# Optimization experiments

Measured on AMD Instinct MI355X. Metric: run time of the kernel, lower is better.

The kernel has to match this reference:

```python
import jax, jax.numpy as jnp
import numpy as np

BETA = 1.0
GAMMA = 0.25


def setup_inputs() -> dict:
    key = jax.random.key(0)
    ks = jax.random.split(key, 8)
    N, D_in, D_h, D_z = 65536, 1024, 512, 256
    s = lambda fan_in: 1.0 / np.sqrt(fan_in)
    return {
        "x": jax.random.normal(ks[0], (N, D_in), jnp.float32),
        "eW1": jax.random.normal(ks[1], (D_in, D_h), jnp.float32) * s(D_in),
        "eb1": jnp.zeros((D_h,), jnp.float32),
        "eW2": jax.random.normal(ks[2], (D_h, D_z), jnp.float32) * s(D_h),
        "eb2": jnp.zeros((D_z,), jnp.float32),
        "dW1": jax.random.normal(ks[3], (D_z, D_h), jnp.float32) * s(D_z),
        "db1": jnp.zeros((D_h,), jnp.float32),
        "dW2": jax.random.normal(ks[4], (D_h, D_in), jnp.float32) * s(D_h),
        "db2": jnp.zeros((D_in,), jnp.float32),
        "C0": jax.random.normal(ks[5], (1024, D_z), jnp.float32),
        "C1": jax.random.normal(ks[6], (512, D_z), jnp.float32),
        "C2": jax.random.normal(ks[7], (256, D_z), jnp.float32),
    }


def _nearest_idx(r, C):
    # argmin of squared euclidean distance == argmin of cdist(p=2)
    r = jax.lax.stop_gradient(r)
    d2 = jnp.sum(r * r, -1, keepdims=True) - 2.0 * (r @ C.T) + jnp.sum(C * C, -1)
    return jnp.argmin(d2, axis=-1)


def reference(x, eW1, eb1, eW2, eb2, dW1, db1, dW2, db2, C0, C1, C2):
    sg = jax.lax.stop_gradient
    # encoder: Linear -> GELU (exact) -> Linear
    z = jax.nn.gelu(x @ eW1 + eb1, approximate=False) @ eW2 + eb2
    residual = z
    output = jnp.zeros_like(z)
    losses = []
    for C in (C0, C1, C2):
        idx = _nearest_idx(residual, sg(C))
        q = C[idx]                                    # [N, 256] gather
        z2c = jnp.mean((residual - sg(q)) ** 2)       # commit input to code
        c2z = jnp.mean((sg(residual) - q) ** 2)       # move code to input
        losses.append(BETA * c2z + GAMMA * z2c)
        output = output + q
        residual = residual - q
    # straight-through: z + sg(zq) - sg(z)
    h = z + sg(output) - sg(z)
    out = jax.nn.gelu(h @ dW1 + db1, approximate=False) @ dW2 + db2
    recon_loss = jnp.mean((out - x) ** 2)
    return jnp.stack([recon_loss] + losses)  # [4]: recon, commit0, commit1, commit2
```

## Files before the change

kernel.cpp:

```cpp
#include <hip/hip_runtime.h>
#include <cstddef>


typedef __attribute__((ext_vector_type(8))) __bf16 bf16x8;
typedef __attribute__((ext_vector_type(4))) float f32x4;
typedef unsigned short u16;

__device__ __forceinline__ u16 f2bf(float f) {
    unsigned u = __float_as_uint(f);
    u += 0x7fffu + ((u >> 16) & 1u);
    return (u16)(u >> 16);
}
__device__ __forceinline__ float bf2f(u16 b) {
    return __uint_as_float((unsigned)b << 16);
}
__device__ __forceinline__ float gelu_exact(float v) {
    return 0.5f * v * (1.0f + erff(v * 0.7071067811865475f));
}
__device__ __forceinline__ void gload16(const void* g, void* l) {
    __builtin_amdgcn_global_load_lds(
        (const __attribute__((address_space(1))) void*)g,
        (__attribute__((address_space(3))) void*)l, 16, 0, 0);
}
__device__ __forceinline__ f32x4 mfma_bf16(bf16x8 a, bf16x8 b, f32x4 c) {
    return __builtin_amdgcn_mfma_f32_16x16x32_bf16(a, b, c, 0, 0, 0);
}

__global__ __launch_bounds__(256)
void prep_x(const float* __restrict__ x, u16* __restrict__ xbf)
{
    const size_t total = (size_t)65536 * 1024;
    const size_t step  = (size_t)gridDim.x * 256 * 8;
    for (size_t i = ((size_t)blockIdx.x * 256 + threadIdx.x) * 8; i < total; i += step) {
        float4 v0 = *(const float4*)&x[i];
        float4 v1 = *(const float4*)&x[i + 4];
        uint4 o;
        o.x = (unsigned)f2bf(v0.x) | ((unsigned)f2bf(v0.y) << 16);
        o.y = (unsigned)f2bf(v0.z) | ((unsigned)f2bf(v0.w) << 16);
        o.z = (unsigned)f2bf(v1.x) | ((unsigned)f2bf(v1.y) << 16);
        o.w = (unsigned)f2bf(v1.z) | ((unsigned)f2bf(v1.w) << 16);
        *(uint4*)&xbf[i] = o;
    }
}

__global__ __launch_bounds__(256)
void prep_weights(const float* __restrict__ eW1, const float* __restrict__ eW2,
                  const float* __restrict__ dW1, const float* __restrict__ dW2,
                  u16* __restrict__ eW1t, u16* __restrict__ eW2t,
                  u16* __restrict__ dW1t, u16* __restrict__ dW2t)
{
    const int b = blockIdx.x, t = threadIdx.x;
    if (b < 2048) {
        int e = b * 256 + t;
        int n = e >> 10, k = e & 1023;
        eW1t[e] = f2bf(eW1[(size_t)k * 512 + n]);
    } else if (b < 2560) {
        int e = (b - 2048) * 256 + t;
        int n = e >> 9, k = e & 511;
        eW2t[e] = f2bf(eW2[(size_t)k * 256 + n]);
    } else if (b < 3072) {
        int e = (b - 2560) * 256 + t;
        int n = e >> 8, k = e & 255;
        dW1t[e] = f2bf(dW1[(size_t)k * 512 + n]);
    } else {
        int e = (b - 3072) * 256 + t;
        int n = e >> 9, k = e & 511;
        dW2t[e] = f2bf(dW2[(size_t)k * 1024 + n]);
    }
}

__global__ __launch_bounds__(256)
void cb_prep(const float* __restrict__ C0, const float* __restrict__ C1,
             const float* __restrict__ C2, u16* __restrict__ Cbf,
             float* __restrict__ cnorm)
{
    __shared__ float red[256];
    const int code = blockIdx.x, t = threadIdx.x;
    const float* C;
    int local;
    if (code < 1024)      { C = C0; local = code; }
    else if (code < 1536) { C = C1; local = code - 1024; }
    else                  { C = C2; local = code - 1536; }
    const float v = C[(size_t)local * 256 + t];
    Cbf[(size_t)code * 256 + t] = f2bf(v);
    red[t] = v * v;
    __syncthreads();
    for (int s = 128; s; s >>= 1) { if (t < s) red[t] += red[t + s]; __syncthreads(); }
    if (t == 0) cnorm[code] = red[0];
}

template <int EPI>
__global__ __launch_bounds__(512, 2)
void gemm_mfma(const u16* __restrict__ A, const u16* __restrict__ Bt,
               const float* __restrict__ bias, u16* __restrict__ Obf,
               float* __restrict__ Of, const u16* __restrict__ Xbf,
               float* __restrict__ lossOut, int N, int K, int ntn,
               float lossScale)
{
    __shared__ __align__(16) u16 SA[2][2][8192];
    __shared__ __align__(16) u16 SB[2][2][8192];

    const int nwg = gridDim.x;
    const int bid = blockIdx.x;
    const int wg  = (bid & 7) * (nwg >> 3) + (bid >> 3);
    const int brow = (wg / ntn) * 256;
    const int bcol = (wg % ntn) * 256;

    const int t    = threadIdx.x;
    const int lane = t & 63;
    const int wid  = t >> 6;
    const int wrow = (wid >> 2) * 128;
    const int wcol = (wid & 3) * 64;
    const int lrow = lane & 15, g = lane >> 4;

    const int nt = K >> 6;

    f32x4 acc[8][4];
#pragma unroll
    for (int m = 0; m < 8; ++m)
#pragma unroll
        for (int n = 0; n < 4; ++n) acc[m][n] = (f32x4)0.f;

    auto stage_half = [&](const u16* __restrict__ src, int row0, int Ts,
                          int kh, char* region) {
#pragma unroll
        for (int it = 0; it < 2; ++it) {
            const int d  = (it * 512 + t) * 16;
            const int R  = d >> 6;
            const int cs = ((d >> 4) & 3) ^ ((R >> 1) & 3);
            gload16(&src[(size_t)(row0 + R) * K + Ts * 64 + kh * 32 + cs * 8],
                    region + d);
        }
    };

    stage_half(A,  brow, 0, 0, (char*)&SA[0][0][0]);
    stage_half(Bt, bcol, 0, 0, (char*)&SB[0][0][0]);
    stage_half(A,  brow, 0, 1, (char*)&SA[0][1][0]);
    stage_half(Bt, bcol, 0, 1, (char*)&SB[0][1][0]);
    stage_half(A,  brow, 1, 0, (char*)&SA[1][0][0]);
    stage_half(Bt, bcol, 1, 0, (char*)&SB[1][0][0]);
    asm volatile("s_waitcnt vmcnt(8)" ::: "memory");
    __builtin_amdgcn_s_barrier();

    bf16x8 bfr[4];

#define PHASE(MH, KK, DO_B, STAGE_CODE)                                        \
    {                                                                          \
        bf16x8 a_[4];                                                          \
        _Pragma("unroll")                                                      \
        for (int mi = 0; mi < 4; ++mi) {                                       \
            const int R = wrow + ((MH) * 4 + mi) * 16 + lrow;                  \
            a_[mi] = *(const bf16x8*)((const char*)&SA[d][KK][0]               \
                      + R * 64 + ((g ^ ((R >> 1) & 3)) << 4));                 \
        }                                                                      \
        if (DO_B) {                                                            \
            _Pragma("unroll")                                                  \
            for (int n = 0; n < 4; ++n) {                                      \
                const int R = wcol + n * 16 + lrow;                            \
                bfr[n] = *(const bf16x8*)((const char*)&SB[d][KK][0]           \
                          + R * 64 + ((g ^ ((R >> 1) & 3)) << 4));             \
            }                                                                  \
        }                                                                      \
        STAGE_CODE;                                                            \
        if (T >= nt - 2) asm volatile("s_waitcnt vmcnt(0)" ::: "memory");      \
        else             asm volatile("s_waitcnt vmcnt(8)" ::: "memory");      \
        __builtin_amdgcn_s_barrier();                                          \
        __builtin_amdgcn_s_setprio(1);                                         \
        _Pragma("unroll")                                                      \
        for (int mi = 0; mi < 4; ++mi)                                         \
            _Pragma("unroll")                                                  \
            for (int n = 0; n < 4; ++n)                                        \
                acc[(MH) * 4 + mi][n] =                                        \
                    mfma_bf16(a_[mi], bfr[n], acc[(MH) * 4 + mi][n]);          \
        __builtin_amdgcn_s_setprio(0);                                         \
        __builtin_amdgcn_s_barrier();                                          \
    }

    for (int T = 0; T < nt; ++T) {
        const int d = T & 1;
        PHASE(0, 0, 1,
              if (T + 1 < nt) stage_half(A, brow, T + 1, 1,
                                         (char*)&SA[(T + 1) & 1][1][0]));
        PHASE(1, 0, 0,
              if (T + 1 < nt) stage_half(Bt, bcol, T + 1, 1,
                                         (char*)&SB[(T + 1) & 1][1][0]));
        PHASE(0, 1, 1,
              if (T + 2 < nt) stage_half(A, brow, T + 2, 0,
                                         (char*)&SA[T & 1][0][0]));
        PHASE(1, 1, 0,
              if (T + 2 < nt) stage_half(Bt, bcol, T + 2, 0,
                                         (char*)&SB[T & 1][0][0]));
    }
#undef PHASE

    int   colN[4];
    float bn[4];
#pragma unroll
    for (int n = 0; n < 4; ++n) {
        colN[n] = bcol + wcol + n * 16 + lrow;
        bn[n]   = bias[colN[n]];
    }

    if (EPI == 0) {
#pragma unroll
        for (int m = 0; m < 8; ++m) {
            const int rowb = brow + wrow + m * 16 + (lane >> 4) * 4;
#pragma unroll
            for (int n = 0; n < 4; ++n)
#pragma unroll
                for (int j = 0; j < 4; ++j)
                    Obf[(size_t)(rowb + j) * N + colN[n]] =
                        f2bf(gelu_exact(acc[m][n][j] + bn[n]));
        }
    } else if (EPI == 1) {
#pragma unroll
        for (int m = 0; m < 8; ++m) {
            const int rowb = brow + wrow + m * 16 + (lane >> 4) * 4;
#pragma unroll
            for (int n = 0; n < 4; ++n)
#pragma unroll
                for (int j = 0; j < 4; ++j)
                    Of[(size_t)(rowb + j) * N + colN[n]] = acc[m][n][j] + bn[n];
        }
    } else if (EPI == 3) {
#pragma unroll
        for (int m = 0; m < 8; ++m) {
            const int rowb = brow + wrow + m * 16 + (lane >> 4) * 4;
#pragma unroll
            for (int n = 0; n < 4; ++n)
#pragma unroll
                for (int j = 0; j < 4; ++j)
                    Obf[(size_t)(rowb + j) * N + colN[n]] =
                        f2bf(acc[m][n][j] + bn[n]);
        }
    } else {
        float partial = 0.f;
#pragma unroll
        for (int m = 0; m < 8; ++m) {
            const int rowb = brow + wrow + m * 16 + (lane >> 4) * 4;
#pragma unroll
            for (int n = 0; n < 4; ++n)
#pragma unroll
                for (int j = 0; j < 4; ++j) {
                    const float o = acc[m][n][j] + bn[n];
                    const float d = o - bf2f(Xbf[(size_t)(rowb + j) * N + colN[n]]);
                    partial = fmaf(d, d, partial);
                }
        }
        __syncthreads();
        float* red = (float*)&SA[0][0][0];
        red[t] = partial;
        __syncthreads();
        for (int s = 256; s; s >>= 1) { if (t < s) red[t] += red[t + s]; __syncthreads(); }
        if (t == 0) atomicAdd(lossOut, red[0] * lossScale);
    }
}

__global__ __launch_bounds__(512, 4)
void vq_mfma(const u16* __restrict__ Zbf, const u16* __restrict__ Cbf,
             const float* __restrict__ cnorm,
             const float* __restrict__ C0, const float* __restrict__ C1,
             const float* __restrict__ C2,
             u16* __restrict__ ZQ, float* __restrict__ lossOut)
{
    __shared__ __align__(16) char pool[66560];
    __shared__ float redv[64][2];
    __shared__ int   redi[64][2];
    __shared__ int   idxs[3][64];
    __shared__ float lred[8];

    u16 (*Rb)[264] = (u16 (*)[264])(pool + 32768);

    const int t    = threadIdx.x;
    const int lane = t & 63;
    const int wid  = t >> 6;
    const int rg   = wid & 3;
    const int cg   = wid >> 2;
    const int lrow = lane & 15, g = lane >> 4;
    const int col  = t & 255;
    const int rh   = t >> 8;
    const int brow = blockIdx.x * 64;

    float R[32];
#pragma unroll
    for (int r = 0; r < 32; ++r)
        R[r] = bf2f(Zbf[(size_t)(brow + rh * 32 + r) * 256 + col]);

    const float* Cf[3]  = {C0, C1, C2};
    const int ncodes[3] = {1024, 512, 256};
    const int coff[3]   = {0, 1024, 1536};
    const float lscale  = 1.25f / (65536.0f * 256.0f);

    const int cr = cg * 16 + lrow;

    for (int stage = 0; stage < 3; ++stage) {
        const u16*   Cb  = Cbf + (size_t)coff[stage] * 256;
        const float* cns = cnorm + coff[stage];
        const int ntile  = ncodes[stage] >> 5;

        auto stageC = [&](int tile) {
            char* region = pool + (size_t)(tile % 3) * 16384;
#pragma unroll
            for (int it = 0; it < 2; ++it) {
                const int d   = (it * 512 + t) * 16;
                const int row = d >> 9;
                const int kb  = d & 511;
                const int kbs = kb ^ ((row & 7) << 4);
                gload16(&Cb[(size_t)(tile * 32 + row) * 256 + (kbs >> 1)],
                        region + d);
            }
        };

        stageC(0);
        if (ntile > 1) stageC(1);
#pragma unroll
        for (int r = 0; r < 32; ++r) Rb[rh * 32 + r][col] = f2bf(R[r]);
        __syncthreads();

        bf16x8 a[8];
#pragma unroll
        for (int ks = 0; ks < 8; ++ks)
            a[ks] = *(const bf16x8*)&Rb[rg * 16 + lrow][ks * 32 + g * 8];
        __syncthreads();

        float best[4]; int bidx[4];
#pragma unroll
        for (int j = 0; j < 4; ++j) { best[j] = 3.0e38f; bidx[j] = 0; }

#pragma unroll 1
        for (int tile = 0; tile < ntile; ++tile) {
            if (tile >= 1) {
                if (tile + 1 < ntile) asm volatile("s_waitcnt vmcnt(2)" ::: "memory");
                else                  asm volatile("s_waitcnt vmcnt(0)" ::: "memory");
                __builtin_amdgcn_s_barrier();
            }
            if (tile + 2 < ntile) stageC(tile + 2);

            const char* Cbuf = pool + (size_t)(tile % 3) * 16384;
            const int   code = tile * 32 + cr;
            const float cn   = cns[code];
            f32x4 acc = (f32x4)0.f;
            __builtin_amdgcn_s_setprio(1);
#pragma unroll
            for (int ks = 0; ks < 8; ++ks) {
                const int kb = (ks * 64 + g * 16) ^ ((cr & 7) << 4);
                bf16x8 b = *(const bf16x8*)(Cbuf + cr * 512 + kb);
                acc = mfma_bf16(a[ks], b, acc);
            }
            __builtin_amdgcn_s_setprio(0);
#pragma unroll
            for (int j = 0; j < 4; ++j) {
                const float s = fmaf(-2.0f, acc[j], cn);
                if (s < best[j]) { best[j] = s; bidx[j] = code; }
            }
        }

#pragma unroll
        for (int j = 0; j < 4; ++j) {
            float v = best[j]; int i = bidx[j];
#pragma unroll
            for (int d = 1; d < 16; d <<= 1) {
                const float ov = __shfl_xor(v, d);
                const int   oi = __shfl_xor(i, d);
                if (ov < v || (ov == v && oi < i)) { v = ov; i = oi; }
            }
            if (lrow == 0) {
                redv[rg * 16 + g * 4 + j][cg] = v;
                redi[rg * 16 + g * 4 + j][cg] = i;
            }
        }
        __syncthreads();
        if (t < 64) {
            float v = redv[t][0]; int i = redi[t][0];
            const float ov = redv[t][1]; const int oi = redi[t][1];
            if (ov < v || (ov == v && oi < i)) { v = ov; i = oi; }
            idxs[stage][t] = i;
        }
        __syncthreads();

        const float* Cfs = Cf[stage];
        float partial = 0.f;
#pragma unroll
        for (int r = 0; r < 32; ++r) {
            const float q  = Cfs[(size_t)idxs[stage][rh * 32 + r] * 256 + col];
            const float rn = R[r] - q;
            R[r] = rn;
            partial = fmaf(rn, rn, partial);
        }
#pragma unroll
        for (int d = 32; d; d >>= 1) partial += __shfl_down(partial, d);
        if (lane == 0) lred[wid] = partial;
        __syncthreads();
        if (t == 0) {
            float s = 0.f;
#pragma unroll
            for (int w2 = 0; w2 < 8; ++w2) s += lred[w2];
            atomicAdd(&lossOut[1 + stage], s * lscale);
        }
        __syncthreads();
    }

#pragma unroll
    for (int r = 0; r < 32; ++r) {
        const int row = rh * 32 + r;
        const float zq = C0[(size_t)idxs[0][row] * 256 + col]
                       + C1[(size_t)idxs[1][row] * 256 + col]
                       + C2[(size_t)idxs[2][row] * 256 + col];
        ZQ[(size_t)(brow + row) * 256 + col] = f2bf(zq);
    }
}

extern "C" void kernel_launch(void* const* d_in, const int* in_sizes, int n_in,
                              void* d_out, int out_size, void* d_ws, size_t ws_size,
                              hipStream_t stream)
{
    const float* x   = (const float*)d_in[0];
    const float* eW1 = (const float*)d_in[1];
    const float* eb1 = (const float*)d_in[2];
    const float* eW2 = (const float*)d_in[3];
    const float* eb2 = (const float*)d_in[4];
    const float* dW1 = (const float*)d_in[5];
    const float* db1 = (const float*)d_in[6];
    const float* dW2 = (const float*)d_in[7];
    const float* db2 = (const float*)d_in[8];
    const float* C0  = (const float*)d_in[9];
    const float* C1  = (const float*)d_in[10];
    const float* C2  = (const float*)d_in[11];
    float* out = (float*)d_out;

    char* w = (char*)d_ws;
    u16*   H1   = (u16*)(w);
    u16*   Zbf  = (u16*)(w + ((size_t)64 << 20));
    u16*   ZQ   = (u16*)(w + ((size_t)128 << 20));
    u16*   H2   = (u16*)(w + ((size_t)160 << 20));
    u16*   xbf  = (u16*)(w + ((size_t)230 << 20));
    u16*   eW1t = (u16*)(w + ((size_t)224 << 20));
    u16*   eW2t = (u16*)(w + ((size_t)225 << 20));
    u16*   dW1t = (u16*)(w + ((size_t)226 << 20));
    u16*   dW2t = (u16*)(w + ((size_t)227 << 20));
    u16*   Cbf  = (u16*)(w + ((size_t)228 << 20));
    float* cn   = (float*)(w + ((size_t)229 << 20));

    hipMemsetAsync(d_out, 0, 4 * sizeof(float), stream);

    prep_x<<<4096, 256, 0, stream>>>(x, xbf);
    prep_weights<<<5120, 256, 0, stream>>>(eW1, eW2, dW1, dW2, eW1t, eW2t, dW1t, dW2t);
    cb_prep<<<1792, 256, 0, stream>>>(C0, C1, C2, Cbf, cn);

    gemm_mfma<0><<<512, 512, 0, stream>>>(
        xbf, eW1t, eb1, H1, nullptr, nullptr, nullptr, 512, 1024, 2, 0.f);
    gemm_mfma<3><<<256, 512, 0, stream>>>(
        H1, eW2t, eb2, Zbf, nullptr, nullptr, nullptr, 256, 512, 1, 0.f);
    vq_mfma<<<1024, 512, 0, stream>>>(Zbf, Cbf, cn, C0, C1, C2, ZQ, out);
    gemm_mfma<0><<<512, 512, 0, stream>>>(
        ZQ, dW1t, db1, H2, nullptr, nullptr, nullptr, 512, 256, 2, 0.f);
    gemm_mfma<2><<<1024, 512, 0, stream>>>(
        H2, dW2t, db2, nullptr, nullptr, xbf, out, 1024, 512, 4,
        1.0f / (65536.0f * 1024.0f));
}
```

Before: 549.9 us.

## Halve VQ block size so each wave computes two row tiles sharing codebook fragments

The VQ kernel now uses 256 threads (4 waves) instead of 512. Each wave handles 32 rows via two 16-row MFMA tiles that share each codebook B fragment loaded from LDS, and each thread keeps 64 residual values in registers. The goal is to halve LDS reads of the codebook per MFMA and raise MFMA density per wave. The cost is higher register pressure, lower launch-bound occupancy (2 blocks) and fewer waves to hide latency in the gather and residual phases.

```diff
diff --git a/kernel.cpp b/kernel.cpp
--- a/kernel.cpp
+++ b/kernel.cpp
@@ -256,7 +256,7 @@
     }
 }
 
-__global__ __launch_bounds__(512, 4)
+__global__ __launch_bounds__(256, 2)
 void vq_mfma(const u16* __restrict__ Zbf, const u16* __restrict__ Cbf,
              const float* __restrict__ cnorm,
              const float* __restrict__ C0, const float* __restrict__ C1,
@@ -267,24 +267,22 @@
     __shared__ float redv[64][2];
     __shared__ int   redi[64][2];
     __shared__ int   idxs[3][64];
-    __shared__ float lred[8];
+    __shared__ float lred[4];
 
     u16 (*Rb)[264] = (u16 (*)[264])(pool + 32768);
 
     const int t    = threadIdx.x;
     const int lane = t & 63;
     const int wid  = t >> 6;
-    const int rg   = wid & 3;
-    const int cg   = wid >> 2;
+    const int rh2  = wid & 1;
+    const int cg   = wid >> 1;
     const int lrow = lane & 15, g = lane >> 4;
-    const int col  = t & 255;
-    const int rh   = t >> 8;
     const int brow = blockIdx.x * 64;
 
-    float R[32];
-#pragma unroll
-    for (int r = 0; r < 32; ++r)
-        R[r] = bf2f(Zbf[(size_t)(brow + rh * 32 + r) * 256 + col]);
+    float R[64];
+#pragma unroll
+    for (int r = 0; r < 64; ++r)
+        R[r] = bf2f(Zbf[(size_t)(brow + r) * 256 + t]);
 
     const float* Cf[3]  = {C0, C1, C2};
     const int ncodes[3] = {1024, 512, 256};
@@ -301,8 +299,8 @@
         auto stageC = [&](int tile) {
             char* region = pool + (size_t)(tile % 3) * 16384;
 #pragma unroll
-            for (int it = 0; it < 2; ++it) {
-                const int d   = (it * 512 + t) * 16;
+            for (int it = 0; it < 4; ++it) {
+                const int d   = (it * 256 + t) * 16;
                 const int row = d >> 9;
                 const int kb  = d & 511;
                 const int kbs = kb ^ ((row & 7) << 4);
@@ -314,23 +312,28 @@
         stageC(0);
         if (ntile > 1) stageC(1);
 #pragma unroll
-        for (int r = 0; r < 32; ++r) Rb[rh * 32 + r][col] = f2bf(R[r]);
-        __syncthreads();
-
-        bf16x8 a[8];
-#pragma unroll
-        for (int ks = 0; ks < 8; ++ks)
-            a[ks] = *(const bf16x8*)&Rb[rg * 16 + lrow][ks * 32 + g * 8];
-        __syncthreads();
-
-        float best[4]; int bidx[4];
-#pragma unroll
-        for (int j = 0; j < 4; ++j) { best[j] = 3.0e38f; bidx[j] = 0; }
+        for (int r = 0; r < 64; ++r) Rb[r][t] = f2bf(R[r]);
+        __syncthreads();
+
+        bf16x8 a0[8], a1[8];
+#pragma unroll
+        for (int ks = 0; ks < 8; ++ks) {
+            a0[ks] = *(const bf16x8*)&Rb[rh2 * 32 + lrow][ks * 32 + g * 8];
+            a1[ks] = *(const bf16x8*)&Rb[rh2 * 32 + 16 + lrow][ks * 32 + g * 8];
+        }
+        __syncthreads();
+
+        float best0[4], best1[4]; int bidx0[4], bidx1[4];
+#pragma unroll
+        for (int j = 0; j < 4; ++j) {
+            best0[j] = 3.0e38f; bidx0[j] = 0;
+            best1[j] = 3.0e38f; bidx1[j] = 0;
+        }
 
 #pragma unroll 1
         for (int tile = 0; tile < ntile; ++tile) {
             if (tile >= 1) {
-                if (tile + 1 < ntile) asm volatile("s_waitcnt vmcnt(2)" ::: "memory");
+                if (tile + 1 < ntile) asm volatile("s_waitcnt vmcnt(4)" ::: "memory");
                 else                  asm volatile("s_waitcnt vmcnt(0)" ::: "memory");
                 __builtin_amdgcn_s_barrier();
             }
@@ -339,34 +342,52 @@
             const char* Cbuf = pool + (size_t)(tile % 3) * 16384;
             const int   code = tile * 32 + cr;
             const float cn   = cns[code];
-            f32x4 acc = (f32x4)0.f;
+            f32x4 acc0 = (f32x4)0.f, acc1 = (f32x4)0.f;
             __builtin_amdgcn_s_setprio(1);
 #pragma unroll
             for (int ks = 0; ks < 8; ++ks) {
                 const int kb = (ks * 64 + g * 16) ^ ((cr & 7) << 4);
                 bf16x8 b = *(const bf16x8*)(Cbuf + cr * 512 + kb);
-                acc = mfma_bf16(a[ks], b, acc);
+                acc0 = mfma_bf16(a0[ks], b, acc0);
+                acc1 = mfma_bf16(a1[ks], b, acc1);
             }
             __builtin_amdgcn_s_setprio(0);
 #pragma unroll
             for (int j = 0; j < 4; ++j) {
-                const float s = fmaf(-2.0f, acc[j], cn);
-                if (s < best[j]) { best[j] = s; bidx[j] = code; }
+                const float s0 = fmaf(-2.0f, acc0[j], cn);
+                if (s0 < best0[j]) { best0[j] = s0; bidx0[j] = code; }
+                const float s1 = fmaf(-2.0f, acc1[j], cn);
+                if (s1 < best1[j]) { best1[j] = s1; bidx1[j] = code; }
             }
         }
 
 #pragma unroll
         for (int j = 0; j < 4; ++j) {
-            float v = best[j]; int i = bidx[j];
-#pragma unroll
-            for (int d = 1; d < 16; d <<= 1) {
-                const float ov = __shfl_xor(v, d);
-                const int   oi = __shfl_xor(i, d);
-                if (ov < v || (ov == v && oi < i)) { v = ov; i = oi; }
-            }
-            if (lrow == 0) {
-                redv[rg * 16 + g * 4 + j][cg] = v;
-                redi[rg * 16 + g * 4 + j][cg] = i;
+            {
+                float v = best0[j]; int i = bidx0[j];
+#pragma unroll
+                for (int d = 1; d < 16; d <<= 1) {
+                    const float ov = __shfl_xor(v, d);
+                    const int   oi = __shfl_xor(i, d);
+                    if (ov < v || (ov == v && oi < i)) { v = ov; i = oi; }
+                }
+                if (lrow == 0) {
+                    redv[rh2 * 32 + g * 4 + j][cg] = v;
+                    redi[rh2 * 32 + g * 4 + j][cg] = i;
+                }
+            }
+            {
+                float v = best1[j]; int i = bidx1[j];
+#pragma unroll
+                for (int d = 1; d < 16; d <<= 1) {
+                    const float ov = __shfl_xor(v, d);
+                    const int   oi = __shfl_xor(i, d);
+                    if (ov < v || (ov == v && oi < i)) { v = ov; i = oi; }
+                }
+                if (lrow == 0) {
+                    redv[rh2 * 32 + 16 + g * 4 + j][cg] = v;
+                    redi[rh2 * 32 + 16 + g * 4 + j][cg] = i;
+                }
             }
         }
         __syncthreads();
@@ -381,8 +402,8 @@
         const float* Cfs = Cf[stage];
         float partial = 0.f;
 #pragma unroll
-        for (int r = 0; r < 32; ++r) {
-            const float q  = Cfs[(size_t)idxs[stage][rh * 32 + r] * 256 + col];
+        for (int r = 0; r < 64; ++r) {
+            const float q  = Cfs[(size_t)idxs[stage][r] * 256 + t];
             const float rn = R[r] - q;
             R[r] = rn;
             partial = fmaf(rn, rn, partial);
@@ -392,21 +413,18 @@
         if (lane == 0) lred[wid] = partial;
         __syncthreads();
         if (t == 0) {
-            float s = 0.f;
-#pragma unroll
-            for (int w2 = 0; w2 < 8; ++w2) s += lred[w2];
+            float s = lred[0] + lred[1] + lred[2] + lred[3];
             atomicAdd(&lossOut[1 + stage], s * lscale);
         }
         __syncthreads();
     }
 
 #pragma unroll
-    for (int r = 0; r < 32; ++r) {
-        const int row = rh * 32 + r;
-        const float zq = C0[(size_t)idxs[0][row] * 256 + col]
-                       + C1[(size_t)idxs[1][row] * 256 + col]
-                       + C2[(size_t)idxs[2][row] * 256 + col];
-        ZQ[(size_t)(brow + row) * 256 + col] = f2bf(zq);
+    for (int r = 0; r < 64; ++r) {
+        const float zq = C0[(size_t)idxs[0][r] * 256 + t]
+                       + C1[(size_t)idxs[1][r] * 256 + t]
+                       + C2[(size_t)idxs[2][r] * 256 + t];
+        ZQ[(size_t)(brow + r) * 256 + t] = f2bf(zq);
     }
 }
 
@@ -451,7 +469,7 @@
         xbf, eW1t, eb1, H1, nullptr, nullptr, nullptr, 512, 1024, 2, 0.f);
     gemm_mfma<3><<<256, 512, 0, stream>>>(
         H1, eW2t, eb2, Zbf, nullptr, nullptr, nullptr, 256, 512, 1, 0.f);
-    vq_mfma<<<1024, 512, 0, stream>>>(Zbf, Cbf, cn, C0, C1, C2, ZQ, out);
+    vq_mfma<<<1024, 256, 0, stream>>>(Zbf, Cbf, cn, C0, C1, C2, ZQ, out);
     gemm_mfma<0><<<512, 512, 0, stream>>>(
         ZQ, dW1t, db1, H2, nullptr, nullptr, nullptr, 512, 256, 2, 0.f);
     gemm_mfma<2><<<1024, 512, 0, stream>>>(
```

New measurement: 613.0 us. 11.5% more time.
